# Kernel tuning notes

Measured on AMD Instinct MI355X. Metric: run time of the kernel, lower is better.

## Reference

```python
import jax, jax.numpy as jnp
import numpy as np

B, S, P, L, H = 64, 512, 32, 30, 768
FH = 1024  # fc_hidden_size


def setup_inputs() -> dict:
    key = jax.random.key(0)
    ks = jax.random.split(key, 8)
    token_embeddings = jax.random.normal(ks[0], (B, S, H), jnp.float32)
    pooler_output = jax.random.normal(ks[1], (B, H), jnp.float32)
    num_positions = jax.random.randint(ks[2], (B, P), 0, S)
    # labels: 0/1 codes, with trailing slots per example padded with -1 rows
    lab = jax.random.randint(ks[3], (B, P, L), 0, 2).astype(jnp.float32)
    valid = jax.random.randint(ks[4], (B, 1), 8, P + 1)  # num real slots per example
    row = jnp.arange(P)[None, :]
    lab = jnp.where((row < valid)[:, :, None], lab, -1.0)
    num_codes_labels = lab.reshape(B, P * L)
    W1 = jax.random.normal(ks[5], (2 * H, FH), jnp.float32) / np.sqrt(2 * H)
    b1 = jnp.zeros((FH,), jnp.float32)
    W2 = jax.random.normal(ks[6], (FH, FH // 2), jnp.float32) / np.sqrt(FH)
    b2 = jnp.zeros((FH // 2,), jnp.float32)
    W3 = jax.random.normal(ks[7], (FH // 2, L), jnp.float32) / np.sqrt(FH // 2)
    b3 = jnp.zeros((L,), jnp.float32)
    return {"token_embeddings": token_embeddings, "pooler_output": pooler_output,
            "num_positions": num_positions, "num_codes_labels": num_codes_labels,
            "W1": W1, "b1": b1, "W2": W2, "b2": b2, "W3": W3, "b3": b3}


def reference(token_embeddings, pooler_output, num_positions, num_codes_labels,
              W1, b1, W2, b2, W3, b3):
    # gather number-token hidden states: [B, P, H]
    p_hidden = jnp.take_along_axis(token_embeddings, num_positions[:, :, None], axis=1)
    feat = jnp.concatenate(
        [p_hidden, jnp.broadcast_to(pooler_output[:, None, :], p_hidden.shape)], axis=-1)
    # Batch_Net_CLS head. NOTE: original uses nn.LeakyReLU(True) -> negative_slope=1.0,
    # which is mathematically the identity, so the activations are omitted (faithful).
    h = feat @ W1 + b1
    h = h @ W2 + b2
    logits = h @ W3 + b3  # [B, P, L]

    labels = num_codes_labels.reshape(B, -1, L)
    pad_pre = jnp.any(labels != -1.0, axis=-1)  # [B, P] True for real slots
    mf = pad_pre.astype(jnp.float32)

    # BCEWithLogitsLoss over non-pad elements: softplus(x) - x*y, mean
    bce_elem = jax.nn.softplus(logits) - logits * labels
    bce_loss = jnp.sum(bce_elem * mf[:, :, None]) / (jnp.sum(mf) * L)

    binary = (jax.nn.sigmoid(logits) > 0.5).astype(jnp.float32)
    count_out = jnp.sum(binary, axis=-1)
    count_lab = jnp.sum(labels, axis=-1)
    count_loss = jnp.mean((count_out - count_lab) ** 2 * mf)

    # position loss: only slots where both counts are exactly 1 (single-hot)
    eq = (count_out == 1.0) & (count_lab == 1.0)
    pos_out = jnp.argmax(binary, axis=-1).astype(jnp.float32)
    pos_lab = jnp.argmax(labels, axis=-1).astype(jnp.float32)
    n_eq = jnp.sum(eq.astype(jnp.float32))
    pos_sum = jnp.sum((pos_out - pos_lab) ** 2 * eq.astype(jnp.float32))
    position_loss = jnp.where(n_eq > 0, pos_sum / jnp.maximum(n_eq, 1.0), 0.0)

    return bce_loss + 10.0 * count_loss + 5.0 * position_loss
```

## Files before the change

### kernel.cpp

```cpp
#include <hip/hip_runtime.h>
#include <cstddef>
#include <cstdint>

#define Mq   2048
#define Lq   30
#define N1q  1024
#define N2q  512
#define K1q  1536
#define Hq   768
#define NBLK 512


__global__ __launch_bounds__(256)
void prep1(const float* __restrict__ W2, const float* __restrict__ W3,
           const float* __restrict__ b2, const float* __restrict__ b3,
           float* __restrict__ W23, float* __restrict__ beff23) {
  const int bid = blockIdx.x, tid = threadIdx.x;
  if (bid < 120) {
    __shared__ float Ws[7680];
    const int idx = bid * 256 + tid;
    const int k = idx / Lq, c = idx - k * Lq;
    const float* w2r = W2 + (size_t)k * N2q;
    float s0 = 0.f, s1 = 0.f, s2 = 0.f, s3 = 0.f;
    for (int half = 0; half < 2; ++half) {
      __syncthreads();
      for (int i = tid * 4; i < 7680; i += 1024)
        *(float4*)&Ws[i] = *(const float4*)&W3[half * 7680 + i];
      __syncthreads();
      const float* w2h = w2r + half * 256;
      #pragma unroll 4
      for (int j = 0; j < 256; j += 4) {
        const float4 wv = *(const float4*)(w2h + j);
        s0 = fmaf(wv.x, Ws[(j    ) * Lq + c], s0);
        s1 = fmaf(wv.y, Ws[(j + 1) * Lq + c], s1);
        s2 = fmaf(wv.z, Ws[(j + 2) * Lq + c], s2);
        s3 = fmaf(wv.w, Ws[(j + 3) * Lq + c], s3);
      }
    }
    W23[idx] = (s0 + s1) + (s2 + s3);
  } else {
    __shared__ float R[8][32];
    const int c = tid % Lq, jc = tid / Lq;
    if (tid < 240) {
      float s = 0.f;
      for (int j = jc * 64; j < jc * 64 + 64; ++j)
        s = fmaf(b2[j], W3[(size_t)j * Lq + c], s);
      R[jc][c] = s;
    }
    __syncthreads();
    if (tid < Lq) {
      float t = b3[tid];
      #pragma unroll
      for (int g = 0; g < 8; ++g) t += R[g][tid];
      beff23[tid] = t;
    }
  }
}

__global__ __launch_bounds__(256)
void prep2(const float* __restrict__ W1, const float* __restrict__ b1,
           const float* __restrict__ W23, const float* __restrict__ beff23,
           float* __restrict__ W123, float* __restrict__ btot) {
  const int bid = blockIdx.x, tid = threadIdx.x;
  if (bid < 180) {
    __shared__ float Ws[7680];
    const int idx = bid * 256 + tid;
    const int k = idx / Lq, c = idx - k * Lq;
    const float* w1r = W1 + (size_t)k * N1q;
    float s0 = 0.f, s1 = 0.f, s2 = 0.f, s3 = 0.f;
    for (int ph = 0; ph < 4; ++ph) {
      __syncthreads();
      for (int i = tid * 4; i < 7680; i += 1024)
        *(float4*)&Ws[i] = *(const float4*)&W23[ph * 7680 + i];
      __syncthreads();
      const float* w1h = w1r + ph * 256;
      #pragma unroll 4
      for (int j = 0; j < 256; j += 4) {
        const float4 wv = *(const float4*)(w1h + j);
        s0 = fmaf(wv.x, Ws[(j    ) * Lq + c], s0);
        s1 = fmaf(wv.y, Ws[(j + 1) * Lq + c], s1);
        s2 = fmaf(wv.z, Ws[(j + 2) * Lq + c], s2);
        s3 = fmaf(wv.w, Ws[(j + 3) * Lq + c], s3);
      }
    }
    W123[idx] = (s0 + s1) + (s2 + s3);
  } else {
    __shared__ float R[8][32];
    const int c = tid % Lq, jc = tid / Lq;
    if (tid < 240) {
      float s = 0.f;
      for (int j = jc * 128; j < jc * 128 + 128; ++j)
        s = fmaf(b1[j], W23[(size_t)j * Lq + c], s);
      R[jc][c] = s;
    }
    __syncthreads();
    if (tid < Lq) {
      float t = beff23[tid];
      #pragma unroll
      for (int g = 0; g < 8; ++g) t += R[g][tid];
      btot[tid] = t;
    }
  }
}

__global__ __launch_bounds__(256)
void loss_kernel(const float* __restrict__ tok, const float* __restrict__ pool,
                 const int* __restrict__ npos, const float* __restrict__ W123,
                 const float* __restrict__ btot, const float* __restrict__ labels,
                 float* __restrict__ part) {
  __shared__ float hrow[4][1536];
  __shared__ float red[4][5];
  const int tid = threadIdx.x, w = tid >> 6, lane = tid & 63;
  const int m = blockIdx.x * 4 + w;
  const int bI = m >> 5, p = m & 31;

  {
    const int pos = npos[bI * 32 + p];
    const float* src1 = tok + ((size_t)bI * 512 + pos) * Hq;
    const float* src2 = pool + (size_t)bI * Hq;
    for (int g = lane; g < 384; g += 64) {
      const float* s = (g < 192) ? (src1 + g * 4) : (src2 + (g - 192) * 4);
      *(float4*)&hrow[w][g * 4] = *(const float4*)s;
    }
  }
  __syncthreads();

  const int c  = lane & 31;
  const int kh = lane >> 5;
  float a0 = 0.f, a1 = 0.f, a2 = 0.f, a3 = 0.f;
  if (c < Lq) {
    const float* hp = hrow[w] + kh * 768;
    const float* wp = W123 + (size_t)(kh * 768) * Lq + c;
    #pragma unroll 4
    for (int i = 0; i < 768; i += 4) {
      a0 = fmaf(hp[i],     wp[(i)     * Lq], a0);
      a1 = fmaf(hp[i + 1], wp[(i + 1) * Lq], a1);
      a2 = fmaf(hp[i + 2], wp[(i + 2) * Lq], a2);
      a3 = fmaf(hp[i + 3], wp[(i + 3) * Lq], a3);
    }
  }
  float a = (a0 + a1) + (a2 + a3);
  a += __shfl_xor(a, 32);

  const bool act = lane < Lq;
  float logit = 0.f, lab = 0.f;
  if (act) {
    logit = a + btot[lane];
    lab = labels[(size_t)m * Lq + lane];
  }

  const unsigned long long validmask = __ballot(act && lab != -1.0f);
  const unsigned long long outmask   = __ballot(act && logit > 0.0f);
  const unsigned long long labmask   = __ballot(act && lab == 1.0f);
  const bool valid = (validmask != 0ULL);
  const int count_out = __popcll(outmask);
  const int count_lab = __popcll(labmask);

  float bce = 0.f;
  if (act && valid) {
    const float x = logit;
    bce = fmaxf(x, 0.f) + log1pf(expf(-fabsf(x))) - x * lab;
  }
  bce += __shfl_xor(bce, 16); bce += __shfl_xor(bce, 8);
  bce += __shfl_xor(bce, 4);  bce += __shfl_xor(bce, 2);
  bce += __shfl_xor(bce, 1);

  if (lane == 0) {
    float pb = 0.f, pv = 0.f, pc = 0.f, pe = 0.f, pp = 0.f;
    if (valid) {
      pb = bce; pv = 1.f;
      const float d = (float)count_out - (float)count_lab;
      pc = d * d;
    }
    if (count_out == 1 && count_lab == 1) {
      const float po = (float)(__ffsll((long long)outmask) - 1);
      const float pl = (float)(__ffsll((long long)labmask) - 1);
      pe = 1.f;
      const float dp = po - pl;
      pp = dp * dp;
    }
    red[w][0] = pb; red[w][1] = pv; red[w][2] = pc; red[w][3] = pe; red[w][4] = pp;
  }
  __syncthreads();
  if (tid < 5) {
    part[blockIdx.x * 5 + tid] =
        red[0][tid] + red[1][tid] + red[2][tid] + red[3][tid];
  }
}

__global__ __launch_bounds__(256)
void finalize_kernel(const float* __restrict__ part, float* __restrict__ out) {
  __shared__ float red[32][5];
  const int t = threadIdx.x;
  if (t < 160) {
    const int j = t % 5, grp = t / 5;
    float s = 0.f;
    for (int i = grp; i < NBLK; i += 32) s += part[i * 5 + j];
    red[grp][j] = s;
  }
  __syncthreads();
  if (t == 0) {
    float t0 = 0.f, t1 = 0.f, t2 = 0.f, t3 = 0.f, t4 = 0.f;
    #pragma unroll
    for (int g = 0; g < 32; ++g) {
      t0 += red[g][0]; t1 += red[g][1]; t2 += red[g][2];
      t3 += red[g][3]; t4 += red[g][4];
    }
    const float bce = t0 / (t1 * (float)Lq);
    const float cnt = 10.0f * t2 / (float)Mq;
    const float pos = (t3 > 0.f) ? 5.0f * t4 / fmaxf(t3, 1.0f) : 0.f;
    out[0] = bce + cnt + pos;
  }
}

extern "C" void kernel_launch(void* const* d_in, const int* in_sizes, int n_in,
                              void* d_out, int out_size, void* d_ws, size_t ws_size,
                              hipStream_t stream) {
  const float* tok    = (const float*)d_in[0];
  const float* pool   = (const float*)d_in[1];
  const int*   npos   = (const int*)  d_in[2];
  const float* labels = (const float*)d_in[3];
  const float* W1     = (const float*)d_in[4];
  const float* b1     = (const float*)d_in[5];
  const float* W2     = (const float*)d_in[6];
  const float* b2     = (const float*)d_in[7];
  const float* W3     = (const float*)d_in[8];
  const float* b3     = (const float*)d_in[9];
  float* out = (float*)d_out;

  char* ws = (char*)d_ws;
  float* W23    = (float*)(ws + 0x00000000);
  float* W123   = (float*)(ws + 0x00020000);
  float* beff23 = (float*)(ws + 0x00050000);
  float* btot   = (float*)(ws + 0x00050200);
  float* part   = (float*)(ws + 0x00051000);

  prep1<<<121, 256, 0, stream>>>(W2, W3, b2, b3, W23, beff23);
  prep2<<<181, 256, 0, stream>>>(W1, b1, W23, beff23, W123, btot);
  loss_kernel<<<NBLK, 256, 0, stream>>>(tok, pool, npos, W123, btot, labels, part);
  finalize_kernel<<<1, 256, 0, stream>>>(part, out);
}
```

Before: 207.6 us.

## Split W2·W3 fold across blocks, prefetch W1 into cache, restructure loss GEMV

prep1 now splits the W2·W3 reduction into two K-halves on separate blocks, writing partial sums that prep2 adds together, which doubles block-level parallelism. Extra blocks in prep1 read all of W1 and discard the result, so W1 is warm in L2/LLC before prep2 runs. The inner loops are unrolled into 16-wide groups. In loss_kernel each wave now handles a K-slice for all four rows, so each W123 load is reused four times, with a shared-memory cross-wave reduction added. The costs are extra workspace, an added barrier and wasted bandwidth if the W1 prefetch does not stay resident.

```diff
diff --git a/kernel.cpp b/kernel.cpp
--- a/kernel.cpp
+++ b/kernel.cpp
@@ -11,34 +11,49 @@
 #define NBLK 512
 
 
+#define G16(P, OFS) do {                                                      \
+  const float4 a0_ = *(const float4*)((P) + (OFS));                           \
+  const float4 a1_ = *(const float4*)((P) + (OFS) + 4);                       \
+  const float4 a2_ = *(const float4*)((P) + (OFS) + 8);                       \
+  const float4 a3_ = *(const float4*)((P) + (OFS) + 12);                      \
+  s0 = fmaf(a0_.x, Ws[((OFS) +  0) * Lq + c], s0);                            \
+  s1 = fmaf(a0_.y, Ws[((OFS) +  1) * Lq + c], s1);                            \
+  s2 = fmaf(a0_.z, Ws[((OFS) +  2) * Lq + c], s2);                            \
+  s3 = fmaf(a0_.w, Ws[((OFS) +  3) * Lq + c], s3);                            \
+  s0 = fmaf(a1_.x, Ws[((OFS) +  4) * Lq + c], s0);                            \
+  s1 = fmaf(a1_.y, Ws[((OFS) +  5) * Lq + c], s1);                            \
+  s2 = fmaf(a1_.z, Ws[((OFS) +  6) * Lq + c], s2);                            \
+  s3 = fmaf(a1_.w, Ws[((OFS) +  7) * Lq + c], s3);                            \
+  s0 = fmaf(a2_.x, Ws[((OFS) +  8) * Lq + c], s0);                            \
+  s1 = fmaf(a2_.y, Ws[((OFS) +  9) * Lq + c], s1);                            \
+  s2 = fmaf(a2_.z, Ws[((OFS) + 10) * Lq + c], s2);                            \
+  s3 = fmaf(a2_.w, Ws[((OFS) + 11) * Lq + c], s3);                            \
+  s0 = fmaf(a3_.x, Ws[((OFS) + 12) * Lq + c], s0);                            \
+  s1 = fmaf(a3_.y, Ws[((OFS) + 13) * Lq + c], s1);                            \
+  s2 = fmaf(a3_.z, Ws[((OFS) + 14) * Lq + c], s2);                            \
+  s3 = fmaf(a3_.w, Ws[((OFS) + 15) * Lq + c], s3);                            \
+} while (0)
+
 __global__ __launch_bounds__(256)
 void prep1(const float* __restrict__ W2, const float* __restrict__ W3,
            const float* __restrict__ b2, const float* __restrict__ b3,
-           float* __restrict__ W23, float* __restrict__ beff23) {
+           const float* __restrict__ W1, float* __restrict__ W23p,
+           float* __restrict__ beff23) {
   const int bid = blockIdx.x, tid = threadIdx.x;
-  if (bid < 120) {
+  if (bid < 240) {
     __shared__ float Ws[7680];
-    const int idx = bid * 256 + tid;
+    const int s   = bid / 120;
+    const int idx = (bid % 120) * 256 + tid;
     const int k = idx / Lq, c = idx - k * Lq;
-    const float* w2r = W2 + (size_t)k * N2q;
+    for (int i = tid * 4; i < 7680; i += 1024)
+      *(float4*)&Ws[i] = *(const float4*)&W3[s * 7680 + i];
+    __syncthreads();
+    const float* w2h = W2 + (size_t)k * N2q + s * 256;
     float s0 = 0.f, s1 = 0.f, s2 = 0.f, s3 = 0.f;
-    for (int half = 0; half < 2; ++half) {
-      __syncthreads();
-      for (int i = tid * 4; i < 7680; i += 1024)
-        *(float4*)&Ws[i] = *(const float4*)&W3[half * 7680 + i];
-      __syncthreads();
-      const float* w2h = w2r + half * 256;
-      #pragma unroll 4
-      for (int j = 0; j < 256; j += 4) {
-        const float4 wv = *(const float4*)(w2h + j);
-        s0 = fmaf(wv.x, Ws[(j    ) * Lq + c], s0);
-        s1 = fmaf(wv.y, Ws[(j + 1) * Lq + c], s1);
-        s2 = fmaf(wv.z, Ws[(j + 2) * Lq + c], s2);
-        s3 = fmaf(wv.w, Ws[(j + 3) * Lq + c], s3);
-      }
-    }
-    W23[idx] = (s0 + s1) + (s2 + s3);
-  } else {
+    #pragma unroll 4
+    for (int j = 0; j < 256; j += 16) G16(w2h, j);
+    W23p[(size_t)s * 30720 + idx] = (s0 + s1) + (s2 + s3);
+  } else if (bid == 240) {
     __shared__ float R[8][32];
     const int c = tid % Lq, jc = tid / Lq;
     if (tid < 240) {
@@ -54,12 +69,20 @@
       for (int g = 0; g < 8; ++g) t += R[g][tid];
       beff23[tid] = t;
     }
+  } else {
+    const float* src = W1 + (size_t)(bid - 241) * 32768;
+    float4 acc = {0.f, 0.f, 0.f, 0.f};
+    for (int i = tid * 4; i < 32768; i += 1024) {
+      const float4 v = *(const float4*)(src + i);
+      acc.x += v.x; acc.y += v.y; acc.z += v.z; acc.w += v.w;
+    }
+    asm volatile("" :: "v"(acc.x), "v"(acc.y), "v"(acc.z), "v"(acc.w));
   }
 }
 
 __global__ __launch_bounds__(256)
 void prep2(const float* __restrict__ W1, const float* __restrict__ b1,
-           const float* __restrict__ W23, const float* __restrict__ beff23,
+           const float* __restrict__ W23p, const float* __restrict__ beff23,
            float* __restrict__ W123, float* __restrict__ btot) {
   const int bid = blockIdx.x, tid = threadIdx.x;
   if (bid < 180) {
@@ -70,18 +93,18 @@
     float s0 = 0.f, s1 = 0.f, s2 = 0.f, s3 = 0.f;
     for (int ph = 0; ph < 4; ++ph) {
       __syncthreads();
-      for (int i = tid * 4; i < 7680; i += 1024)
-        *(float4*)&Ws[i] = *(const float4*)&W23[ph * 7680 + i];
+      for (int i = tid * 4; i < 7680; i += 1024) {
+        const float4 p0 = *(const float4*)&W23p[ph * 7680 + i];
+        const float4 p1 = *(const float4*)&W23p[30720 + ph * 7680 + i];
+        float4 sm;
+        sm.x = p0.x + p1.x; sm.y = p0.y + p1.y;
+        sm.z = p0.z + p1.z; sm.w = p0.w + p1.w;
+        *(float4*)&Ws[i] = sm;
+      }
       __syncthreads();
       const float* w1h = w1r + ph * 256;
       #pragma unroll 4
-      for (int j = 0; j < 256; j += 4) {
-        const float4 wv = *(const float4*)(w1h + j);
-        s0 = fmaf(wv.x, Ws[(j    ) * Lq + c], s0);
-        s1 = fmaf(wv.y, Ws[(j + 1) * Lq + c], s1);
-        s2 = fmaf(wv.z, Ws[(j + 2) * Lq + c], s2);
-        s3 = fmaf(wv.w, Ws[(j + 3) * Lq + c], s3);
-      }
+      for (int j = 0; j < 256; j += 16) G16(w1h, j);
     }
     W123[idx] = (s0 + s1) + (s2 + s3);
   } else {
@@ -90,7 +113,8 @@
     if (tid < 240) {
       float s = 0.f;
       for (int j = jc * 128; j < jc * 128 + 128; ++j)
-        s = fmaf(b1[j], W23[(size_t)j * Lq + c], s);
+        s = fmaf(b1[j],
+                 W23p[(size_t)j * Lq + c] + W23p[30720 + (size_t)j * Lq + c], s);
       R[jc][c] = s;
     }
     __syncthreads();
@@ -109,12 +133,14 @@
                  const float* __restrict__ btot, const float* __restrict__ labels,
                  float* __restrict__ part) {
   __shared__ float hrow[4][1536];
+  __shared__ float red2[4][4][32];
   __shared__ float red[4][5];
   const int tid = threadIdx.x, w = tid >> 6, lane = tid & 63;
-  const int m = blockIdx.x * 4 + w;
-  const int bI = m >> 5, p = m & 31;
+  const int mbase = blockIdx.x * 4;
 
   {
+    const int m = mbase + w;
+    const int bI = m >> 5, p = m & 31;
     const int pos = npos[bI * 32 + p];
     const float* src1 = tok + ((size_t)bI * 512 + pos) * Hq;
     const float* src2 = pool + (size_t)bI * Hq;
@@ -129,23 +155,37 @@
   const int kh = lane >> 5;
   float a0 = 0.f, a1 = 0.f, a2 = 0.f, a3 = 0.f;
   if (c < Lq) {
-    const float* hp = hrow[w] + kh * 768;
-    const float* wp = W123 + (size_t)(kh * 768) * Lq + c;
+    const int k0 = w * 384 + kh * 192;
+    const float* wp = W123 + (size_t)k0 * Lq + c;
+    const float* h0 = &hrow[0][k0];
+    const float* h1 = &hrow[1][k0];
+    const float* h2 = &hrow[2][k0];
+    const float* h3 = &hrow[3][k0];
     #pragma unroll 4
-    for (int i = 0; i < 768; i += 4) {
-      a0 = fmaf(hp[i],     wp[(i)     * Lq], a0);
-      a1 = fmaf(hp[i + 1], wp[(i + 1) * Lq], a1);
-      a2 = fmaf(hp[i + 2], wp[(i + 2) * Lq], a2);
-      a3 = fmaf(hp[i + 3], wp[(i + 3) * Lq], a3);
-    }
-  }
-  float a = (a0 + a1) + (a2 + a3);
-  a += __shfl_xor(a, 32);
-
+    for (int i = 0; i < 192; ++i) {
+      const float wv = wp[(size_t)i * Lq];
+      a0 = fmaf(h0[i], wv, a0);
+      a1 = fmaf(h1[i], wv, a1);
+      a2 = fmaf(h2[i], wv, a2);
+      a3 = fmaf(h3[i], wv, a3);
+    }
+  }
+  a0 += __shfl_xor(a0, 32);
+  a1 += __shfl_xor(a1, 32);
+  a2 += __shfl_xor(a2, 32);
+  a3 += __shfl_xor(a3, 32);
+  if (lane < Lq) {
+    red2[w][0][lane] = a0; red2[w][1][lane] = a1;
+    red2[w][2][lane] = a2; red2[w][3][lane] = a3;
+  }
+  __syncthreads();
+
+  const int m = mbase + w;
   const bool act = lane < Lq;
   float logit = 0.f, lab = 0.f;
   if (act) {
-    logit = a + btot[lane];
+    logit = red2[0][w][lane] + red2[1][w][lane] + red2[2][w][lane]
+          + red2[3][w][lane] + btot[lane];
     lab = labels[(size_t)m * Lq + lane];
   }
 
@@ -229,14 +269,14 @@
   float* out = (float*)d_out;
 
   char* ws = (char*)d_ws;
-  float* W23    = (float*)(ws + 0x00000000);
-  float* W123   = (float*)(ws + 0x00020000);
-  float* beff23 = (float*)(ws + 0x00050000);
-  float* btot   = (float*)(ws + 0x00050200);
-  float* part   = (float*)(ws + 0x00051000);
-
-  prep1<<<121, 256, 0, stream>>>(W2, W3, b2, b3, W23, beff23);
-  prep2<<<181, 256, 0, stream>>>(W1, b1, W23, beff23, W123, btot);
+  float* W23p   = (float*)(ws + 0x00000000);
+  float* W123   = (float*)(ws + 0x00040000);
+  float* beff23 = (float*)(ws + 0x00070000);
+  float* btot   = (float*)(ws + 0x00070200);
+  float* part   = (float*)(ws + 0x00071000);
+
+  prep1<<<289, 256, 0, stream>>>(W2, W3, b2, b3, W1, W23p, beff23);
+  prep2<<<181, 256, 0, stream>>>(W1, b1, W23p, beff23, W123, btot);
   loss_kernel<<<NBLK, 256, 0, stream>>>(tok, pool, npos, W123, btot, labels, part);
   finalize_kernel<<<1, 256, 0, stream>>>(part, out);
 }
```

Result: no change. 207.9 us (+0.2%).
